# Kernel tuning notes

Measured on AMD Instinct MI355X. Metric: run time of the kernel, lower is better.

The kernel has to match this reference:

```python
import jax, jax.numpy as jnp
import numpy as np

E = 768      # embed_size
H = 12       # num_heads inside each nn.MultiheadAttention
G = 4        # num_groups
D = E // H   # per-head dim = 64


def setup_inputs() -> dict:
    key = jax.random.key(0)
    ks = jax.random.split(key, 20)
    s = 0.02
    B, S = 2, 2048
    inp = {
        "query": jax.random.normal(ks[0], (B, S, E), jnp.float32),
        "key":   jax.random.normal(ks[1], (B, S, E), jnp.float32),
        "value": jax.random.normal(ks[2], (B, S, E), jnp.float32),
        # outer projections (query_group_proj / key_proj / value_proj)
        "Wqg": jax.random.normal(ks[3], (E, E), jnp.float32) * s,
        "bqg": jnp.zeros((E,), jnp.float32),
        "Wk":  jax.random.normal(ks[4], (E, E), jnp.float32) * s,
        "bk":  jnp.zeros((E,), jnp.float32),
        "Wv":  jax.random.normal(ks[5], (E, E), jnp.float32) * s,
        "bv":  jnp.zeros((E,), jnp.float32),
        # per-group MultiheadAttention params (in_proj split into q/k/v, out_proj)
        "Wq_in": jax.random.normal(ks[6], (G, E, E), jnp.float32) * s,
        "bq_in": jnp.zeros((G, E), jnp.float32),
        "Wk_in": jax.random.normal(ks[7], (G, E, E), jnp.float32) * s,
        "bk_in": jnp.zeros((G, E), jnp.float32),
        "Wv_in": jax.random.normal(ks[8], (G, E, E), jnp.float32) * s,
        "bv_in": jnp.zeros((G, E), jnp.float32),
        "Wout":  jax.random.normal(ks[9], (G, E, E), jnp.float32) * s,
        "bout":  jnp.zeros((G, E), jnp.float32),
    }
    return inp


def reference(query, key, value, Wqg, bqg, Wk, bk, Wv, bv,
              Wq_in, bq_in, Wk_in, bk_in, Wv_in, bv_in, Wout, bout):
    B, S, _ = query.shape
    T = S // G  # tokens per group
    scale = 1.0 / np.sqrt(D).astype(np.float32)

    # outer projections (Linear: x @ W.T + b)
    q = query @ Wqg.T + bqg                         # [B,S,E]
    k = key   @ Wk.T  + bk                          # [B,S,E]
    v = value @ Wv.T  + bv                          # [B,S,E]

    # split query tokens into G interleaved groups (view + permute in source)
    qg = q.reshape(B, T, G, E).transpose(0, 2, 1, 3)  # [B,G,T,E]

    # per-group MHA input projections (batched over groups)
    qi = jnp.einsum('bgte,gfe->bgtf', qg, Wq_in) + bq_in[None, :, None, :]
    ki = jnp.einsum('bse,gfe->bgsf', k,  Wk_in) + bk_in[None, :, None, :]
    vi = jnp.einsum('bse,gfe->bgsf', v,  Wv_in) + bv_in[None, :, None, :]

    qh = qi.reshape(B, G, T, H, D)
    kh = ki.reshape(B, G, S, H, D)
    vh = vi.reshape(B, G, S, H, D)

    scores = jnp.einsum('bgthd,bgshd->bghts', qh, kh) * scale  # [B,G,H,T,S]
    attn = jax.nn.softmax(scores, axis=-1)
    ctx = jnp.einsum('bghts,bgshd->bgthd', attn, vh).reshape(B, G, T, E)

    out_g = jnp.einsum('bgte,gfe->bgtf', ctx, Wout) + bout[None, :, None, :]  # [B,G,T,E]

    # reassemble sequence order (inverse of the grouping permutation)
    out = out_g.transpose(0, 2, 1, 3).reshape(B, S, E)
    return out
```

## Files before the change

### kernel.cpp

```cpp
#include <hip/hip_runtime.h>
#include <hip/hip_bf16.h>


typedef __attribute__((ext_vector_type(8))) short short8;
typedef __attribute__((ext_vector_type(4))) float floatx4;

static __device__ __forceinline__ short f2bf(float f) {
    __bf16 b = (__bf16)f;
    return __builtin_bit_cast(short, b);
}
static __device__ __forceinline__ short8 f8_to_bf8(floatx4 f0, floatx4 f1) {
    short8 s;
    s[0]=f2bf(f0[0]); s[1]=f2bf(f0[1]); s[2]=f2bf(f0[2]); s[3]=f2bf(f0[3]);
    s[4]=f2bf(f1[0]); s[5]=f2bf(f1[1]); s[6]=f2bf(f1[2]); s[7]=f2bf(f1[3]);
    return s;
}
static __device__ __forceinline__ void gload_lds16(const short* g, short* l) {
    __builtin_amdgcn_global_load_lds(
        (const __attribute__((address_space(1))) unsigned int*)g,
        (__attribute__((address_space(3))) unsigned int*)l, 16, 0, 0);
}

__global__ __launch_bounds__(256) void cast_w(
    const float* a0, const float* a1, const float* a2, const float* a3,
    const float* a4, const float* a5, const float* a6, short* dst)
{
    const long U = 589824L;
    const float* ptrs[7] = {a0,a1,a2,a3,a4,a5,a6};
    const long starts[8] = {0, U, 2*U, 3*U, 7*U, 11*U, 15*U, 19*U};
    long i = (long)blockIdx.x * 2048 + (long)threadIdx.x * 8;
    int t = 0;
    while (t < 6 && i >= starts[t + 1]) t++;
    const float* s = ptrs[t] + (i - starts[t]);
    floatx4 f0 = *(const floatx4*)s;
    floatx4 f1 = *(const floatx4*)(s + 4);
    *(short8*)(dst + i) = f8_to_bf8(f0, f1);
}

#define GEMM_LANE_VARS                                                        \
    const int tid = threadIdx.x, lane = tid & 63, w = tid >> 6;               \
    const int wm = w & 1, wn = w >> 1;                                        \
    const int qr = lane >> 4, lc = lane & 15, x7 = lc & 7;                    \
    const int srow = tid >> 3, schunk = tid & 7, sx = srow & 7;

template<int CMODE, int BIAS_MODE>
static __device__ __forceinline__ void gemm_epilogue(
    floatx4 (&acc)[4][4], const float* bp, void* Cv, int ldc, int bm, int bn,
    int wm, int wn, int qr, int lc)
{
#pragma unroll
    for (int ni = 0; ni < 4; ni++) {
        const int gcol = bn * 128 + wn * 64 + ni * 16 + lc;
        const float bcol = (BIAS_MODE == 0) ? bp[gcol] : 0.f;
#pragma unroll
        for (int mi = 0; mi < 4; mi++) {
#pragma unroll
            for (int r = 0; r < 4; r++) {
                const int grow = bm * 128 + wm * 64 + mi * 16 + qr * 4 + r;
                const float bb = (BIAS_MODE == 1) ? bp[grow] : bcol;
                const float v = acc[mi][ni][r] + bb;
                if (CMODE == 0)
                    ((short*)Cv)[(long)grow * ldc + gcol] = f2bf(v);
                else
                    ((float*)Cv)[(long)grow * ldc + gcol] = v;
            }
        }
    }
}

static __device__ __forceinline__ void gemm_mfma_step(
    floatx4 (&acc)[4][4], const short* Ac, const short* Bc,
    int wm, int wn, int qr, int lc, int x7)
{
#pragma unroll
    for (int ks = 0; ks < 64; ks += 32) {
        const int c0 = (ks >> 3) + qr;
        const int slot = ((c0 ^ x7) << 3);
        short8 af[4], bfr[4];
#pragma unroll
        for (int mi = 0; mi < 4; mi++)
            af[mi] = *(const short8*)&Ac[(wm * 64 + mi * 16 + lc) * 64 + slot];
#pragma unroll
        for (int ni = 0; ni < 4; ni++)
            bfr[ni] = *(const short8*)&Bc[(wn * 64 + ni * 16 + lc) * 64 + slot];
#pragma unroll
        for (int mi = 0; mi < 4; mi++)
#pragma unroll
            for (int ni = 0; ni < 4; ni++)
                acc[mi][ni] = __builtin_amdgcn_mfma_f32_16x16x32_bf16(
                    af[mi], bfr[ni], acc[mi][ni], 0, 0, 0);
    }
}

template<int CMODE, int BIAS_MODE>
static __device__ __forceinline__ void gemm_core_db(
    const short* __restrict__ A, const short* __restrict__ Wb,
    const float* __restrict__ bp, void* __restrict__ Cv,
    int lda, int ldc, int bm, int bn, short* As, short* Bs)
{
    GEMM_LANE_VARS
    const short* Ab = A + (long)(bm * 128) * lda;
    const short* Wt = Wb + (long)(bn * 128) * 768;
    const int gch = ((schunk ^ sx) << 3);

    floatx4 acc[4][4];
#pragma unroll
    for (int mi = 0; mi < 4; mi++)
#pragma unroll
        for (int ni = 0; ni < 4; ni++) acc[mi][ni] = (floatx4){0.f, 0.f, 0.f, 0.f};

#pragma unroll
    for (int p = 0; p < 4; p++) {
        gload_lds16(Ab + (long)(p * 32 + srow) * lda + gch, &As[(p * 32 + w * 8) * 64]);
        gload_lds16(Wt + (long)(p * 32 + srow) * 768 + gch, &Bs[(p * 32 + w * 8) * 64]);
    }

    for (int kk = 0; kk < 12; kk++) {
        __syncthreads();
        if (kk < 11) {
            const int k1 = (kk + 1) * 64;
            const int nb = ((kk + 1) & 1) * 8192;
#pragma unroll
            for (int p = 0; p < 4; p++) {
                gload_lds16(Ab + (long)(p * 32 + srow) * lda + k1 + gch,
                            &As[nb + (p * 32 + w * 8) * 64]);
                gload_lds16(Wt + (long)(p * 32 + srow) * 768 + k1 + gch,
                            &Bs[nb + (p * 32 + w * 8) * 64]);
            }
        }
        gemm_mfma_step(acc, As + (kk & 1) * 8192, Bs + (kk & 1) * 8192,
                       wm, wn, qr, lc, x7);
    }
    gemm_epilogue<CMODE, BIAS_MODE>(acc, bp, Cv, ldc, bm, bn, wm, wn, qr, lc);
}

template<int CMODE, int BIAS_MODE>
static __device__ __forceinline__ void gemm_core_f32(
    const float* __restrict__ A, const short* __restrict__ Wb,
    const float* __restrict__ bp, void* __restrict__ Cv,
    int lda, int ldc, int bm, int bn, short* As, short* Bs)
{
    GEMM_LANE_VARS
    const short* Wt = Wb + (long)(bn * 128) * 768;

    floatx4 acc[4][4];
#pragma unroll
    for (int mi = 0; mi < 4; mi++)
#pragma unroll
        for (int ni = 0; ni < 4; ni++) acc[mi][ni] = (floatx4){0.f, 0.f, 0.f, 0.f};

    for (int k0 = 0; k0 < 768; k0 += 64) {
        __syncthreads();
#pragma unroll
        for (int p = 0; p < 4; p++) {
            const int row = p * 32 + srow;
            const float* ap = A + (long)(bm * 128 + row) * lda + k0 + schunk * 8;
            floatx4 f0 = *(const floatx4*)ap;
            floatx4 f1 = *(const floatx4*)(ap + 4);
            *(short8*)&As[row * 64 + ((schunk ^ sx) << 3)] = f8_to_bf8(f0, f1);
            gload_lds16(Wt + (long)row * 768 + k0 + ((schunk ^ sx) << 3),
                        &Bs[(p * 32 + w * 8) * 64]);
        }
        __syncthreads();
        gemm_mfma_step(acc, As, Bs, wm, wn, qr, lc, x7);
    }
    gemm_epilogue<CMODE, BIAS_MODE>(acc, bp, Cv, ldc, bm, bn, wm, wn, qr, lc);
}

__global__ __launch_bounds__(256) void qkv_gemm(
    const float* q, const float* k, const float* v, const short* Wbf,
    const float* bq, const float* bk, const float* bv, short* outp)
{
    __shared__ short As[128 * 64];
    __shared__ short Bs[128 * 64];
    const int xcd = blockIdx.x & 7, slot = blockIdx.x >> 3;
    const int bm = xcd * 4 + slot / 18;
    const int rem = slot % 18, y = rem / 6, bn = rem % 6;
    const float* A    = (y == 0) ? q  : (y == 1) ? k  : v;
    const float* bias = (y == 0) ? bq : (y == 1) ? bk : bv;
    gemm_core_f32<0, 0>(A, Wbf + (long)y * 589824, bias, outp + (long)y * 3145728,
                        768, 768, bm, bn, As, Bs);
}

template<int BIAS_MODE>
static __device__ __forceinline__ void gemm256_core(
    const short* __restrict__ A, const short* __restrict__ B,
    const float* __restrict__ bias, short* __restrict__ C,
    int lda, int ldc, int bm, int bn, short* As, short* Bs)
{
    const int tid = threadIdx.x, lane = tid & 63, w = tid >> 6;
    const int wm = w & 1, wn = w >> 1;
    const int qr = lane >> 4, lc = lane & 15, x7 = lc & 7;
    const int srow = tid >> 3, schunk = tid & 7;
    const int gch = ((schunk ^ (srow & 7)) << 3);

    const short* Ab = A + (long)(bm * 256) * lda;
    const short* Bb = B + (long)(bn * 256) * 768;

    floatx4 acc[8][4];
#pragma unroll
    for (int i = 0; i < 8; i++)
#pragma unroll
        for (int j = 0; j < 4; j++) acc[i][j] = (floatx4){0.f, 0.f, 0.f, 0.f};

#pragma unroll
    for (int r = 0; r < 256; r += 64) {
        gload_lds16(Ab + (long)(r + srow) * lda + gch, As + (r + w * 8) * 64);
        gload_lds16(Bb + (long)(r + srow) * 768 + gch, Bs + (r + w * 8) * 64);
    }

#pragma unroll 1
    for (int kt = 0; kt < 12; ++kt) {
        const int s = kt & 1;
        const short* Ac = As + s * 16384;
        const short* Bc = Bs + s * 16384;
        short* Ad = As + (1 - s) * 16384;
        short* Bd = Bs + (1 - s) * 16384;
        const int koff = (kt + 1) * 64;

        asm volatile("s_waitcnt vmcnt(0)" ::: "memory");
        __builtin_amdgcn_s_barrier();

        short8 af[4][2], bfr[2][2];
#pragma unroll
        for (int ph = 0; ph < 4; ++ph) {
            const int mh = ph >> 1, nh = ph & 1;
            if (nh == 0) {
#pragma unroll
                for (int mi = 0; mi < 4; mi++)
#pragma unroll
                    for (int ks = 0; ks < 2; ks++)
                        af[mi][ks] = *(const short8*)&Ac[
                            (wm * 128 + (mh * 4 + mi) * 16 + lc) * 64 +
                            ((((ks << 2) + qr) ^ x7) << 3)];
            }
#pragma unroll
            for (int ni = 0; ni < 2; ni++)
#pragma unroll
                for (int ks = 0; ks < 2; ks++)
                    bfr[ni][ks] = *(const short8*)&Bc[
                        (wn * 64 + (nh * 2 + ni) * 16 + lc) * 64 +
                        ((((ks << 2) + qr) ^ x7) << 3)];
            if (kt < 11) {
                const int r = ph * 64;
                gload_lds16(Ab + (long)(r + srow) * lda + koff + gch,
                            Ad + (r + w * 8) * 64);
                gload_lds16(Bb + (long)(r + srow) * 768 + koff + gch,
                            Bd + (r + w * 8) * 64);
            }
            __builtin_amdgcn_s_barrier();
            asm volatile("s_waitcnt lgkmcnt(0)" ::: "memory");
            __builtin_amdgcn_sched_barrier(0);
            __builtin_amdgcn_s_setprio(1);
#pragma unroll
            for (int ks = 0; ks < 2; ks++)
#pragma unroll
                for (int mi = 0; mi < 4; mi++)
#pragma unroll
                    for (int ni = 0; ni < 2; ni++)
                        acc[mh * 4 + mi][nh * 2 + ni] =
                            __builtin_amdgcn_mfma_f32_16x16x32_bf16(
                                af[mi][ks], bfr[ni][ks],
                                acc[mh * 4 + mi][nh * 2 + ni], 0, 0, 0);
            __builtin_amdgcn_s_setprio(0);
            __builtin_amdgcn_sched_barrier(0);
            __builtin_amdgcn_s_barrier();
        }
    }

#pragma unroll
    for (int ni = 0; ni < 4; ni++) {
        const int gcol = bn * 256 + wn * 64 + ni * 16 + lc;
        const float bcol = (BIAS_MODE == 0) ? bias[gcol] : 0.f;
#pragma unroll
        for (int mi = 0; mi < 8; mi++) {
#pragma unroll
            for (int r = 0; r < 4; r++) {
                const int grow = bm * 256 + wm * 128 + mi * 16 + qr * 4 + r;
                const float bb = (BIAS_MODE == 1) ? bias[grow] : bcol;
                C[(long)grow * ldc + gcol] = f2bf(acc[mi][ni][r] + bb);
            }
        }
    }
}

__global__ __launch_bounds__(512, 2) void mid_gemm2(
    const short* kproj, const short* vproj, const short* qproj, const short* Wbf,
    const float* bq_in, const float* bk_in, const float* bv_in,
    short* kiB, short* vtB, short* qiB)
{
    __shared__ short As[2 * 16384];
    __shared__ short Bs[2 * 16384];
    const int xcd = blockIdx.x & 7, slot = blockIdx.x >> 3;
    const int z = xcd, b = z >> 2, g = z & 3;
    if (slot < 24) {
        gemm256_core<0>(kproj + (long)b * 1572864, Wbf + (long)(7 + g) * 589824,
                        bk_in + g * 768, kiB + (long)z * 1572864,
                        768, 768, slot / 3, slot % 3, As, Bs);
    } else if (slot < 48) {
        const int s2 = slot - 24;
        gemm256_core<1>(Wbf + (long)(11 + g) * 589824, vproj + (long)b * 1572864,
                        bv_in + g * 768, vtB + (long)z * 1572864,
                        768, 2048, s2 / 8, s2 % 8, As, Bs);
    } else {
        const int s3 = slot - 48;
        gemm256_core<0>(qproj + (long)b * 1572864 + g * 768, Wbf + (long)(3 + g) * 589824,
                        bq_in + g * 768, qiB + (long)z * 393216,
                        3072, 768, s3 / 3, s3 % 3, As, Bs);
    }
}

__global__ __launch_bounds__(256) void out_gemm(
    const short* ctxB, const short* Wbf, const float* bout, float* out)
{
    extern __shared__ short sm[];
    short* As = sm;
    short* Bs = sm + 16384;
    const int xcd = blockIdx.x & 7, slot = blockIdx.x >> 3;
    const int z = xcd, b = z >> 2, g = z & 3;
    gemm_core_db<2, 0>(ctxB + (long)z * 393216, Wbf + (long)(15 + g) * 589824,
                       bout + g * 768, out + (long)b * 1572864 + g * 768,
                       768, 3072, slot / 6, slot % 6, As, Bs);
}

__global__ __launch_bounds__(256) void attn_kernel(
    const short* __restrict__ qi, const short* __restrict__ ki,
    const short* __restrict__ vt, short* __restrict__ ctx)
{
    __shared__ short Kt[2][64 * 64];
    __shared__ short Vt[2][64 * 64];
    __shared__ short Ps[4][16 * 64];

    const int tid = threadIdx.x, lane = tid & 63, w = tid >> 6;
    const int qr = lane >> 4, lc = lane & 15, x7 = lc & 7;
    const int headid = blockIdx.x % 96;
    const int tile = blockIdx.x / 96;
    const int h = headid % 12, bg = headid / 12;

    const short* qp = qi + ((long)bg * 512 + tile * 64 + w * 16 + lc) * 768 + h * 64 + qr * 8;
    const short8 aq0 = *(const short8*)qp;
    const short8 aq1 = *(const short8*)(qp + 32);

    const short one = (lc == 0) ? (short)0x3F80 : (short)0;
    const short8 onesv = (short8){one, one, one, one, one, one, one, one};

    floatx4 cacc[4], lacc = (floatx4){0.f, 0.f, 0.f, 0.f};
#pragma unroll
    for (int dc = 0; dc < 4; dc++) cacc[dc] = (floatx4){0.f, 0.f, 0.f, 0.f};

    const int srow = lane >> 3, schk = lane & 7, swz = schk ^ srow;
    const short* kgb = ki + ((long)bg * 2048) * 768 + h * 64;
    const short* vgb = vt + ((long)(bg * 768 + h * 64)) * 2048;

#pragma unroll
    for (int inst = 0; inst < 2; inst++) {
        const int rk = w * 16 + inst * 8 + srow;
        gload_lds16(kgb + (long)rk * 768 + swz * 8, &Kt[0][(w * 16 + inst * 8) * 64]);
        gload_lds16(vgb + (long)rk * 2048 + swz * 8, &Vt[0][(w * 16 + inst * 8) * 64]);
    }

    for (int it = 0; it < 32; it++) {
        const int cur = it & 1;
        __syncthreads();
        if (it < 31) {
            const int nxt = cur ^ 1, s0 = (it + 1) * 64;
#pragma unroll
            for (int inst = 0; inst < 2; inst++) {
                const int rk = w * 16 + inst * 8 + srow;
                gload_lds16(kgb + (long)(s0 + rk) * 768 + swz * 8,
                            &Kt[nxt][(w * 16 + inst * 8) * 64]);
                gload_lds16(vgb + (long)rk * 2048 + s0 + swz * 8,
                            &Vt[nxt][(w * 16 + inst * 8) * 64]);
            }
        }

        const short* Kb = &Kt[cur][0];
        const short* Vb = &Vt[cur][0];

        floatx4 sv[4];
        __builtin_amdgcn_s_setprio(1);
#pragma unroll
        for (int ss = 0; ss < 4; ss++) {
            const short* kr = Kb + (ss * 16 + lc) * 64;
            short8 b0 = *(const short8*)(kr + ((qr ^ x7) << 3));
            short8 b1 = *(const short8*)(kr + (((4 + qr) ^ x7) << 3));
            floatx4 t = (floatx4){0.f, 0.f, 0.f, 0.f};
            t = __builtin_amdgcn_mfma_f32_16x16x32_bf16(aq0, b0, t, 0, 0, 0);
            t = __builtin_amdgcn_mfma_f32_16x16x32_bf16(aq1, b1, t, 0, 0, 0);
            sv[ss] = t;
        }
        __builtin_amdgcn_s_setprio(0);

        short* ps = &Ps[w][0];
#pragma unroll
        for (int ss = 0; ss < 4; ss++) {
            const int cch = ss * 2 + (lc >> 3);
#pragma unroll
            for (int r = 0; r < 4; r++) {
                const int m = qr * 4 + r;
                ps[m * 64 + ((cch ^ (m & 7)) << 3) + x7] =
                    f2bf(__builtin_amdgcn_exp2f(sv[ss][r] * 0.18033688f));
            }
        }
        asm volatile("s_waitcnt lgkmcnt(0)" ::: "memory");
        const short8 ap0 = *(const short8*)&ps[lc * 64 + ((qr ^ x7) << 3)];
        const short8 ap1 = *(const short8*)&ps[lc * 64 + (((4 + qr) ^ x7) << 3)];

        __builtin_amdgcn_s_setprio(1);
        lacc = __builtin_amdgcn_mfma_f32_16x16x32_bf16(ap0, onesv, lacc, 0, 0, 0);
        lacc = __builtin_amdgcn_mfma_f32_16x16x32_bf16(ap1, onesv, lacc, 0, 0, 0);
#pragma unroll
        for (int dc = 0; dc < 4; dc++) {
            const short* vr = Vb + (dc * 16 + lc) * 64;
            short8 bv0 = *(const short8*)(vr + ((qr ^ x7) << 3));
            short8 bv1 = *(const short8*)(vr + (((4 + qr) ^ x7) << 3));
            cacc[dc] = __builtin_amdgcn_mfma_f32_16x16x32_bf16(ap0, bv0, cacc[dc], 0, 0, 0);
            cacc[dc] = __builtin_amdgcn_mfma_f32_16x16x32_bf16(ap1, bv1, cacc[dc], 0, 0, 0);
        }
        __builtin_amdgcn_s_setprio(0);
    }

    float linv[4];
#pragma unroll
    for (int r = 0; r < 4; r++)
        linv[r] = 1.f / __shfl(lacc[r], lane & 48);
    short* cp = ctx + ((long)bg * 512 + tile * 64 + w * 16) * 768 + h * 64;
#pragma unroll
    for (int dc = 0; dc < 4; dc++)
#pragma unroll
        for (int r = 0; r < 4; r++)
            cp[(qr * 4 + r) * 768 + dc * 16 + lc] = f2bf(cacc[dc][r] * linv[r]);
}

extern "C" void kernel_launch(void* const* d_in, const int* in_sizes, int n_in,
                              void* d_out, int out_size, void* d_ws, size_t ws_size,
                              hipStream_t stream) {
    const float* query = (const float*)d_in[0];
    const float* key   = (const float*)d_in[1];
    const float* value = (const float*)d_in[2];
    const float* Wqg = (const float*)d_in[3];  const float* bqg = (const float*)d_in[4];
    const float* Wk  = (const float*)d_in[5];  const float* bk  = (const float*)d_in[6];
    const float* Wv  = (const float*)d_in[7];  const float* bv  = (const float*)d_in[8];
    const float* Wq_in = (const float*)d_in[9];  const float* bq_in = (const float*)d_in[10];
    const float* Wk_in = (const float*)d_in[11]; const float* bk_in = (const float*)d_in[12];
    const float* Wv_in = (const float*)d_in[13]; const float* bv_in = (const float*)d_in[14];
    const float* Wout  = (const float*)d_in[15]; const float* bout  = (const float*)d_in[16];
    float* out = (float*)d_out;

    short* ws     = (short*)d_ws;
    short* Wbf    = ws;
    short* q_proj = ws + 11206656L;
    short* k_proj = ws + 14352384L;
    short* v_proj = ws + 17498112L;
    short* qiB    = ws + 20643840L;
    short* vtB    = ws + 23789568L;
    short* kiB    = ws + 36372480L;
    short* ctxB   = ws + 11206656L;

    dim3 blk(256);

    cast_w<<<dim3(5472), blk, 0, stream>>>(
        Wqg, Wk, Wv, Wq_in, Wk_in, Wv_in, Wout, Wbf);

    qkv_gemm<<<dim3(576), blk, 0, stream>>>(
        query, key, value, Wbf, bqg, bk, bv, q_proj);

    mid_gemm2<<<dim3(432), dim3(512), 0, stream>>>(
        k_proj, v_proj, q_proj, Wbf, bq_in, bk_in, bv_in, kiB, vtB, qiB);

    attn_kernel<<<dim3(768), blk, 0, stream>>>(qiB, kiB, vtB, ctxB);

    out_gemm<<<dim3(192), blk, 65536, stream>>>(ctxB, Wbf, bout, out);
}
```

Before: 298.1 us.

## Keep attention probabilities in registers via transposed QK and permuted K rows

```diff
diff --git a/kernel.cpp b/kernel.cpp
--- a/kernel.cpp
+++ b/kernel.cpp
@@ -4,6 +4,7 @@
 
 typedef __attribute__((ext_vector_type(8))) short short8;
 typedef __attribute__((ext_vector_type(4))) float floatx4;
+typedef __attribute__((ext_vector_type(4))) int intx4;
 
 static __device__ __forceinline__ short f2bf(float f) {
     __bf16 b = (__bf16)f;
@@ -14,6 +15,11 @@
     s[0]=f2bf(f0[0]); s[1]=f2bf(f0[1]); s[2]=f2bf(f0[2]); s[3]=f2bf(f0[3]);
     s[4]=f2bf(f1[0]); s[5]=f2bf(f1[1]); s[6]=f2bf(f1[2]); s[7]=f2bf(f1[3]);
     return s;
+}
+static __device__ __forceinline__ unsigned cvt_pk_bf16(float a, float b) {
+    unsigned r;
+    asm("v_cvt_pk_bf16_f32 %0, %1, %2" : "=v"(r) : "v"(a), "v"(b));
+    return r;
 }
 static __device__ __forceinline__ void gload_lds16(const short* g, short* l) {
     __builtin_amdgcn_global_load_lds(
@@ -329,7 +335,6 @@
 {
     __shared__ short Kt[2][64 * 64];
     __shared__ short Vt[2][64 * 64];
-    __shared__ short Ps[4][16 * 64];
 
     const int tid = threadIdx.x, lane = tid & 63, w = tid >> 6;
     const int qr = lane >> 4, lc = lane & 15, x7 = lc & 7;
@@ -341,10 +346,8 @@
     const short8 aq0 = *(const short8*)qp;
     const short8 aq1 = *(const short8*)(qp + 32);
 
-    const short one = (lc == 0) ? (short)0x3F80 : (short)0;
-    const short8 onesv = (short8){one, one, one, one, one, one, one, one};
-
-    floatx4 cacc[4], lacc = (floatx4){0.f, 0.f, 0.f, 0.f};
+    floatx4 cacc[4];
+    float lsum = 0.f;
 #pragma unroll
     for (int dc = 0; dc < 4; dc++) cacc[dc] = (floatx4){0.f, 0.f, 0.f, 0.f};
 
@@ -352,11 +355,16 @@
     const short* kgb = ki + ((long)bg * 2048) * 768 + h * 64;
     const short* vgb = vt + ((long)(bg * 768 + h * 64)) * 2048;
 
-#pragma unroll
-    for (int inst = 0; inst < 2; inst++) {
-        const int rk = w * 16 + inst * 8 + srow;
-        gload_lds16(kgb + (long)rk * 768 + swz * 8, &Kt[0][(w * 16 + inst * 8) * 64]);
-        gload_lds16(vgb + (long)rk * 2048 + swz * 8, &Vt[0][(w * 16 + inst * 8) * 64]);
+#define KPERM(d) ((((d) >> 5) & 1) * 32 + (((d) >> 2) & 3) * 8 + (((d) >> 4) & 1) * 4 + ((d) & 3))
+    const int d0 = w * 16 + srow, d1 = d0 + 8;
+    const int kp0 = KPERM(d0), kp1 = KPERM(d1);
+#undef KPERM
+
+    {
+        gload_lds16(kgb + (long)kp0 * 768 + swz * 8, &Kt[0][(w * 16) * 64]);
+        gload_lds16(kgb + (long)kp1 * 768 + swz * 8, &Kt[0][(w * 16 + 8) * 64]);
+        gload_lds16(vgb + (long)d0 * 2048 + swz * 8, &Vt[0][(w * 16) * 64]);
+        gload_lds16(vgb + (long)d1 * 2048 + swz * 8, &Vt[0][(w * 16 + 8) * 64]);
     }
 
     for (int it = 0; it < 32; it++) {
@@ -364,14 +372,10 @@
         __syncthreads();
         if (it < 31) {
             const int nxt = cur ^ 1, s0 = (it + 1) * 64;
-#pragma unroll
-            for (int inst = 0; inst < 2; inst++) {
-                const int rk = w * 16 + inst * 8 + srow;
-                gload_lds16(kgb + (long)(s0 + rk) * 768 + swz * 8,
-                            &Kt[nxt][(w * 16 + inst * 8) * 64]);
-                gload_lds16(vgb + (long)rk * 2048 + s0 + swz * 8,
-                            &Vt[nxt][(w * 16 + inst * 8) * 64]);
-            }
+            gload_lds16(kgb + (long)(s0 + kp0) * 768 + swz * 8, &Kt[nxt][(w * 16) * 64]);
+            gload_lds16(kgb + (long)(s0 + kp1) * 768 + swz * 8, &Kt[nxt][(w * 16 + 8) * 64]);
+            gload_lds16(vgb + (long)d0 * 2048 + s0 + swz * 8, &Vt[nxt][(w * 16) * 64]);
+            gload_lds16(vgb + (long)d1 * 2048 + s0 + swz * 8, &Vt[nxt][(w * 16 + 8) * 64]);
         }
 
         const short* Kb = &Kt[cur][0];
@@ -385,30 +389,35 @@
             short8 b0 = *(const short8*)(kr + ((qr ^ x7) << 3));
             short8 b1 = *(const short8*)(kr + (((4 + qr) ^ x7) << 3));
             floatx4 t = (floatx4){0.f, 0.f, 0.f, 0.f};
-            t = __builtin_amdgcn_mfma_f32_16x16x32_bf16(aq0, b0, t, 0, 0, 0);
-            t = __builtin_amdgcn_mfma_f32_16x16x32_bf16(aq1, b1, t, 0, 0, 0);
+            t = __builtin_amdgcn_mfma_f32_16x16x32_bf16(b0, aq0, t, 0, 0, 0);
+            t = __builtin_amdgcn_mfma_f32_16x16x32_bf16(b1, aq1, t, 0, 0, 0);
             sv[ss] = t;
         }
         __builtin_amdgcn_s_setprio(0);
 
-        short* ps = &Ps[w][0];
-#pragma unroll
-        for (int ss = 0; ss < 4; ss++) {
-            const int cch = ss * 2 + (lc >> 3);
-#pragma unroll
-            for (int r = 0; r < 4; r++) {
-                const int m = qr * 4 + r;
-                ps[m * 64 + ((cch ^ (m & 7)) << 3) + x7] =
-                    f2bf(__builtin_amdgcn_exp2f(sv[ss][r] * 0.18033688f));
-            }
-        }
-        asm volatile("s_waitcnt lgkmcnt(0)" ::: "memory");
-        const short8 ap0 = *(const short8*)&ps[lc * 64 + ((qr ^ x7) << 3)];
-        const short8 ap1 = *(const short8*)&ps[lc * 64 + (((4 + qr) ^ x7) << 3)];
+        float p[4][4];
+#pragma unroll
+        for (int ss = 0; ss < 4; ss++)
+#pragma unroll
+            for (int r = 0; r < 4; r++)
+                p[ss][r] = __builtin_amdgcn_exp2f(sv[ss][r] * 0.18033688f);
+#pragma unroll
+        for (int ss = 0; ss < 4; ss++)
+            lsum += (p[ss][0] + p[ss][1]) + (p[ss][2] + p[ss][3]);
+
+        intx4 i0, i1;
+        i0[0] = (int)cvt_pk_bf16(p[0][0], p[0][1]);
+        i0[1] = (int)cvt_pk_bf16(p[0][2], p[0][3]);
+        i0[2] = (int)cvt_pk_bf16(p[1][0], p[1][1]);
+        i0[3] = (int)cvt_pk_bf16(p[1][2], p[1][3]);
+        i1[0] = (int)cvt_pk_bf16(p[2][0], p[2][1]);
+        i1[1] = (int)cvt_pk_bf16(p[2][2], p[2][3]);
+        i1[2] = (int)cvt_pk_bf16(p[3][0], p[3][1]);
+        i1[3] = (int)cvt_pk_bf16(p[3][2], p[3][3]);
+        const short8 ap0 = __builtin_bit_cast(short8, i0);
+        const short8 ap1 = __builtin_bit_cast(short8, i1);
 
         __builtin_amdgcn_s_setprio(1);
-        lacc = __builtin_amdgcn_mfma_f32_16x16x32_bf16(ap0, onesv, lacc, 0, 0, 0);
-        lacc = __builtin_amdgcn_mfma_f32_16x16x32_bf16(ap1, onesv, lacc, 0, 0, 0);
 #pragma unroll
         for (int dc = 0; dc < 4; dc++) {
             const short* vr = Vb + (dc * 16 + lc) * 64;
@@ -420,10 +429,13 @@
         __builtin_amdgcn_s_setprio(0);
     }
 
+    lsum += __shfl_xor(lsum, 16);
+    lsum += __shfl_xor(lsum, 32);
     float linv[4];
 #pragma unroll
     for (int r = 0; r < 4; r++)
-        linv[r] = 1.f / __shfl(lacc[r], lane & 48);
+        linv[r] = 1.f / __shfl(lsum, qr * 4 + r);
+
     short* cp = ctx + ((long)bg * 512 + tile * 64 + w * 16) * 768 + h * 64;
 #pragma unroll
     for (int dc = 0; dc < 4; dc++)
```

After: 289.8 us. 2.8% less time.
